# Kernel tuning notes

Measured on AMD Instinct MI355X. Metric: run time of the kernel, lower is better.

The kernel has to match this reference:

```python
import jax, jax.numpy as jnp
import numpy as np

N = 50000   # nodes
E = 800000  # edges
F = 64      # num_node_features
H = 64      # hidden_channels
NB = 3      # num_blocks
G = 64      # graphs in batch
C = 10      # num_classes
EPS = 1e-5  # BatchNorm eps


def setup_inputs() -> dict:
    key = jax.random.key(0)
    ks = jax.random.split(key, 24)
    x = jax.random.normal(ks[0], (N, F), dtype=jnp.float32)
    edge_index = jax.random.randint(ks[1], (2, E), 0, N, dtype=jnp.int64)
    batch = jnp.sort(jax.random.randint(ks[2], (N,), 0, G, dtype=jnp.int64))
    s = 0.05
    inp = {
        "x": x, "edge_index": edge_index, "batch": batch,
        "pre_w": jax.random.normal(ks[3], (F, H)) * s,
        "pre_b": jnp.zeros((H,), jnp.float32),
        # stacked per-block params (blocks are structurally identical)
        "blk_prelu1": jnp.full((NB,), 0.25, jnp.float32),
        "blk_bn_gamma": jnp.ones((NB, H), jnp.float32),
        "blk_bn_beta": jnp.zeros((NB, H), jnp.float32),
        "blk_w1": jax.random.normal(ks[4], (NB, H, 2 * H)) * s,
        "blk_b1": jnp.zeros((NB, 2 * H), jnp.float32),
        "blk_prelu2": jnp.full((NB,), 0.25, jnp.float32),
        "blk_w2": jax.random.normal(ks[5], (NB, 2 * H, H)) * s,
        "blk_b2": jnp.zeros((NB, H), jnp.float32),
        "post_bn_gamma": jnp.ones((H,), jnp.float32),
        "post_bn_beta": jnp.zeros((H,), jnp.float32),
        "fc1_w": jax.random.normal(ks[6], (H, 4 * H)) * s,
        "fc1_b": jnp.zeros((4 * H,), jnp.float32),
        "post_prelu": jnp.asarray(0.25, jnp.float32),
        "fc2_w": jax.random.normal(ks[7], (4 * H, C)) * s,
        "fc2_b": jnp.zeros((C,), jnp.float32),
    }
    return inp


def _prelu(x, a):
    return jnp.where(x >= 0, x, a * x)


def _batchnorm(x, gamma, beta):
    # training-mode BN over the node dimension (biased variance), as in torch
    mean = jnp.mean(x, axis=0)
    var = jnp.var(x, axis=0)
    return (x - mean) * jax.lax.rsqrt(var + EPS) * gamma + beta


def _gcn_conv(x, W, bias, src, dst):
    # PyG GCNConv: linear transform, then D^-1/2 (A+I) D^-1/2 aggregation, then bias.
    h = x @ W                                   # [N, out]
    deg = jax.ops.segment_sum(jnp.ones((E,), h.dtype), dst, num_segments=N) + 1.0
    dinv = jax.lax.rsqrt(deg)                   # [N]
    norm = dinv[src] * dinv[dst]                # [E]
    agg = jax.ops.segment_sum(h[src] * norm[:, None], dst, num_segments=N)
    agg = agg + h * (dinv * dinv)[:, None]      # self-loop contribution
    return agg + bias


def reference(x, edge_index, batch, pre_w, pre_b,
              blk_prelu1, blk_bn_gamma, blk_bn_beta, blk_w1, blk_b1,
              blk_prelu2, blk_w2, blk_b2,
              post_bn_gamma, post_bn_beta, fc1_w, fc1_b, post_prelu, fc2_w, fc2_b):
    src, dst = edge_index[0], edge_index[1]
    h = x @ pre_w + pre_b                       # [N, H]
    for i in range(NB):
        h = _prelu(h, blk_prelu1[i])
        h = _batchnorm(h, blk_bn_gamma[i], blk_bn_beta[i])
        h = _gcn_conv(h, blk_w1[i], blk_b1[i], src, dst)   # [N, 2H]
        h = _prelu(h, blk_prelu2[i])
        h = _gcn_conv(h, blk_w2[i], blk_b2[i], src, dst)   # [N, H]
    # global mean pool per graph
    sums = jax.ops.segment_sum(h, batch, num_segments=G)   # [G, H]
    cnts = jax.ops.segment_sum(jnp.ones((N,), h.dtype), batch, num_segments=G)
    pooled = sums / jnp.maximum(cnts, 1.0)[:, None]
    out = _batchnorm(pooled, post_bn_gamma, post_bn_beta)
    out = out @ fc1_w + fc1_b
    out = _prelu(out, post_prelu)
    # dropout with p=0.0 is identity
    out = out @ fc2_w + fc2_b                   # [G, C]
    return out
```

## Files before the change

### kernel.cpp

```cpp
#include <hip/hip_runtime.h>
#include <hip/hip_fp16.h>

#define NN 50000
#define NE 800000
#define NG 64
#define NC 10
#define BN_EPS 1e-5f
#define NSB 196

typedef __attribute__((ext_vector_type(2))) _Float16 h2v;
typedef __attribute__((ext_vector_type(8))) _Float16 f16x8;
typedef __attribute__((ext_vector_type(4))) float f32x4;

__device__ __forceinline__ float2 up2(unsigned u) {
    __half2 h = *reinterpret_cast<__half2*>(&u);
    return __half22float2(h);
}
__device__ __forceinline__ unsigned pk2(float a, float b) {
    __half2 h = __floats2half2_rn(a, b);
    return *reinterpret_cast<unsigned*>(&h);
}


__global__ void deg_count_kernel(const int* __restrict__ dst, int* __restrict__ deg,
                                 unsigned short* __restrict__ pos16) {
    int e = blockIdx.x * blockDim.x + threadIdx.x;
    if (e < NE) {
        int d = __builtin_nontemporal_load(&dst[e]);
        unsigned short p = (unsigned short)atomicAdd(&deg[d], 1);
        __builtin_nontemporal_store(p, &pos16[e]);
    }
}

__global__ __launch_bounds__(256) void block_sum_kernel(const int* __restrict__ deg,
                                                        int* __restrict__ bsum) {
    int b = blockIdx.x, t = threadIdx.x;
    int n = b * 256 + t;
    int v = (n < NN) ? deg[n] : 0;
    __shared__ int red[256];
    red[t] = v;
    __syncthreads();
    for (int off = 128; off > 0; off >>= 1) {
        if (t < off) red[t] += red[t + off];
        __syncthreads();
    }
    if (t == 0) bsum[b] = red[0];
}

__global__ __launch_bounds__(256) void bsum_scan_kernel(const int* __restrict__ bsum,
                                                        int* __restrict__ boff) {
    __shared__ int s[256];
    int t = threadIdx.x;
    int v = (t < NSB) ? bsum[t] : 0;
    s[t] = v;
    __syncthreads();
    for (int off = 1; off < 256; off <<= 1) {
        int cur = s[t];
        int add = (t >= off) ? s[t - off] : 0;
        __syncthreads();
        s[t] = cur + add;
        __syncthreads();
    }
    if (t < NSB) boff[t] = s[t] - v;
}

__global__ __launch_bounds__(256) void csr_setup_kernel(const int* __restrict__ deg,
                                                        const int* __restrict__ boff,
                                                        int* __restrict__ row_off,
                                                        float* __restrict__ dinv,
                                                        float* __restrict__ rdeg) {
    int b = blockIdx.x, t = threadIdx.x;
    int n = b * 256 + t;
    int v = (n < NN) ? deg[n] : 0;
    __shared__ int s[256];
    s[t] = v;
    __syncthreads();
    for (int off = 1; off < 256; off <<= 1) {
        int cur = s[t];
        int add = (t >= off) ? s[t - off] : 0;
        __syncthreads();
        s[t] = cur + add;
        __syncthreads();
    }
    int excl = s[t] - v + boff[b];
    if (n < NN) {
        row_off[n] = excl;
        float d = (float)v + 1.0f;
        dinv[n] = rsqrtf(d);
        rdeg[n] = sqrtf(d);
    }
    if (n == NN - 1) row_off[NN] = NE;
}

__global__ void scatter_pass_kernel(const int* __restrict__ src, const int* __restrict__ dst,
                                    const unsigned short* __restrict__ pos16,
                                    const int* __restrict__ row_off,
                                    int* __restrict__ csr_src, int d0, int d1) {
    int e = blockIdx.x * blockDim.x + threadIdx.x;
    if (e >= NE) return;
    int d = __builtin_nontemporal_load(&dst[e]);
    if (d < d0 || d >= d1) return;
    int s = __builtin_nontemporal_load(&src[e]);
    int p = (int)__builtin_nontemporal_load(&pos16[e]);
    csr_src[row_off[d] + p] = s;
}

__global__ void arow_kernel(const int* __restrict__ row_off, const int* __restrict__ csr_src,
                            const float* __restrict__ dinv, float* __restrict__ arow) {
    int n = blockIdx.x * 256 + threadIdx.x;
    if (n >= NN) return;
    float dv = dinv[n];
    float s = dv;
    int e0 = row_off[n], e1 = row_off[n + 1];
    for (int i = e0; i < e1; ++i) s += dinv[csr_src[i]];
    arow[n] = dv * s;
}


__global__ __launch_bounds__(256) void bn_stats_kernel(const __half* __restrict__ h,
                                                       const float* __restrict__ rdeg,
                                                       const float* __restrict__ alpha_p,
                                                       float* __restrict__ stats) {
    float alpha = alpha_p[0];
    int tid = threadIdx.x;
    int cg0 = tid & 7;
    int c8 = cg0 * 8;
    int rg = tid >> 3;
    float sm[8], sq[8];
#pragma unroll
    for (int k = 0; k < 8; ++k) { sm[k] = 0.f; sq[k] = 0.f; }
    for (int n = blockIdx.x * 32 + rg; n < NN; n += gridDim.x * 32) {
        float rd = rdeg[n];
        uint4 u = *(const uint4*)&h[(size_t)n * 64 + c8];
        float2 p0 = up2(u.x), p1 = up2(u.y), p2 = up2(u.z), p3 = up2(u.w);
        float e[8] = {p0.x, p0.y, p1.x, p1.y, p2.x, p2.y, p3.x, p3.y};
#pragma unroll
        for (int k = 0; k < 8; ++k) {
            float a = e[k] >= 0.f ? e[k] : alpha * e[k];
            a *= rd;
            sm[k] += a;
            sq[k] += a * a;
        }
    }
    __shared__ float ls[256 * 17];
    float* p = &ls[tid * 17];
#pragma unroll
    for (int k = 0; k < 8; ++k) { p[k] = sm[k]; p[8 + k] = sq[k]; }
    __syncthreads();
    if (tid < 128) {
        int cg = tid >> 4;
        int j = tid & 15;
        float acc = 0.f;
        for (int r = 0; r < 32; ++r) acc += ls[(r * 8 + cg) * 17 + j];
        int ch = cg * 8 + (j & 7);
        atomicAdd(&stats[(j < 8 ? 0 : 64) + ch], acc);
    }
}


template <bool PRELU, int OUT>
__global__ __launch_bounds__(256) void gather_kernel(const int* __restrict__ row_off,
                                                     const int* __restrict__ csr_src,
                                                     const float* __restrict__ dinv,
                                                     const float* __restrict__ bias,
                                                     const float* __restrict__ alpha_p,
                                                     const __half* __restrict__ hh,
                                                     __half* __restrict__ outp) {
    int tid = threadIdx.x;
    int r = blockIdx.x * 32 + (tid >> 3);
    int c = (tid & 7) * 8;
    if (r >= NN) return;
    float alpha = 0.f;
    if constexpr (PRELU) alpha = alpha_p[0];
    float acc[8];
    {
        uint4 u0 = *(const uint4*)&hh[(size_t)r * 64 + c];
        float2 p0 = up2(u0.x), p1 = up2(u0.y), p2 = up2(u0.z), p3 = up2(u0.w);
        acc[0] = p0.x; acc[1] = p0.y; acc[2] = p1.x; acc[3] = p1.y;
        acc[4] = p2.x; acc[5] = p2.y; acc[6] = p3.x; acc[7] = p3.y;
        if constexpr (PRELU) {
#pragma unroll
            for (int k = 0; k < 8; ++k) acc[k] = acc[k] >= 0.f ? acc[k] : alpha * acc[k];
        }
    }
    int beg = row_off[r];
    int end = row_off[r + 1];
    int nct = (end - beg + 7) >> 3;
    int base = beg;
    int q[8];
    if (nct > 0) {
#pragma unroll
        for (int j = 0; j < 8; ++j) {
            int pos = base + j;
            q[j] = csr_src[pos < end ? pos : end - 1];
        }
    }
    for (int it = 0; it < nct; ++it) {
        int s[8];
#pragma unroll
        for (int j = 0; j < 8; ++j) s[j] = q[j];
        int cbase = base;
        base += 8;
        if (it + 1 < nct) {
#pragma unroll
            for (int j = 0; j < 8; ++j) {
                int pos = base + j;
                q[j] = csr_src[pos < end ? pos : end - 1];
            }
        }
        uint4 v[8];
#pragma unroll
        for (int j = 0; j < 8; ++j) v[j] = *(const uint4*)&hh[(size_t)s[j] * 64 + c];
#pragma unroll
        for (int j = 0; j < 8; ++j) {
            float m = (cbase + j < end) ? 1.f : 0.f;
            float2 p0 = up2(v[j].x), p1 = up2(v[j].y), p2 = up2(v[j].z), p3 = up2(v[j].w);
            float e[8] = {p0.x, p0.y, p1.x, p1.y, p2.x, p2.y, p3.x, p3.y};
            if constexpr (PRELU) {
#pragma unroll
                for (int k = 0; k < 8; ++k) e[k] = e[k] >= 0.f ? e[k] : alpha * e[k];
            }
#pragma unroll
            for (int k = 0; k < 8; ++k) acc[k] = fmaf(e[k], m, acc[k]);
        }
    }
    float dv = dinv[r];
    float o[8];
    if constexpr (OUT == 2) {
#pragma unroll
        for (int k = 0; k < 8; ++k) o[k] = dv * acc[k];
    } else {
        float4 b0 = *(const float4*)&bias[c];
        float4 b1 = *(const float4*)&bias[c + 4];
        float bl[8] = {b0.x, b0.y, b0.z, b0.w, b1.x, b1.y, b1.z, b1.w};
#pragma unroll
        for (int k = 0; k < 8; ++k) o[k] = dv * acc[k] + bl[k];
        if constexpr (OUT == 1) {
#pragma unroll
            for (int k = 0; k < 8; ++k) o[k] *= dv;
        }
    }
    uint4 ov;
    ov.x = pk2(o[0], o[1]);
    ov.y = pk2(o[2], o[3]);
    ov.z = pk2(o[4], o[5]);
    ov.w = pk2(o[6], o[7]);
    *(uint4*)&outp[(size_t)r * 64 + c] = ov;
}


__global__ __launch_bounds__(256) void mfma_pre_kernel(const float* __restrict__ x,
                                                       const float* __restrict__ W,
                                                       __half* __restrict__ outp,
                                                       const float* __restrict__ bias,
                                                       const float* __restrict__ dinv) {
    __shared__ _Float16 At[128][72];
    __shared__ _Float16 Wt[64][72];
    int tid = threadIdx.x;
    for (int i = tid; i < 64 * 32; i += 256) {
        int j = i & 63;
        int k2 = i >> 6;
        *(unsigned*)&Wt[j][2 * k2] = pk2(W[(2 * k2) * 64 + j], W[(2 * k2 + 1) * 64 + j]);
    }
    int r0 = blockIdx.x * 128;
    for (int i = tid; i < 128 * 16; i += 256) {
        int row = i >> 4;
        int k4 = (i & 15) * 4;
        int rr = r0 + row;
        if (rr > NN - 1) rr = NN - 1;
        float4 v = *(const float4*)&x[(size_t)rr * 64 + k4];
        *(unsigned*)&At[row][k4]     = pk2(v.x, v.y);
        *(unsigned*)&At[row][k4 + 2] = pk2(v.z, v.w);
    }
    __syncthreads();
    int w = tid >> 6;
    int l = tid & 63;
    int lr = l & 15;
    int lk = (l >> 4) * 8;
    f32x4 acc[2][4];
#pragma unroll
    for (int rt = 0; rt < 2; ++rt)
#pragma unroll
        for (int ct = 0; ct < 4; ++ct) acc[rt][ct] = (f32x4){0.f, 0.f, 0.f, 0.f};
#pragma unroll
    for (int k0 = 0; k0 < 64; k0 += 32) {
        f16x8 a0 = *(const f16x8*)&At[w * 32 + lr][k0 + lk];
        f16x8 a1 = *(const f16x8*)&At[w * 32 + 16 + lr][k0 + lk];
#pragma unroll
        for (int ct = 0; ct < 4; ++ct) {
            f16x8 b = *(const f16x8*)&Wt[ct * 16 + lr][k0 + lk];
            acc[0][ct] = __builtin_amdgcn_mfma_f32_16x16x32_f16(a0, b, acc[0][ct], 0, 0, 0);
            acc[1][ct] = __builtin_amdgcn_mfma_f32_16x16x32_f16(a1, b, acc[1][ct], 0, 0, 0);
        }
    }
    int rowbase = r0 + w * 32 + (l >> 4) * 4;
#pragma unroll
    for (int rt = 0; rt < 2; ++rt) {
#pragma unroll
        for (int ct = 0; ct < 4; ++ct) {
            int col = ct * 16 + lr;
            float bb = bias[col];
#pragma unroll
            for (int r = 0; r < 4; ++r) {
                int row = rowbase + rt * 16 + r;
                if (row < NN)
                    outp[(size_t)row * 64 + col] = __float2half((acc[rt][ct][r] + bb) * dinv[row]);
            }
        }
    }
}


__global__ __launch_bounds__(256) void mfma_mlp_kernel(__half* __restrict__ t,
                                                       const float* __restrict__ W1,
                                                       const float* __restrict__ b1,
                                                       const float* __restrict__ W2,
                                                       const float* __restrict__ alpha2_p,
                                                       const float* __restrict__ stats,
                                                       const float* __restrict__ gamma,
                                                       const float* __restrict__ beta,
                                                       const float* __restrict__ arow,
                                                       const float* __restrict__ dinv) {
    __shared__ __align__(16) char smem[45056];
    auto Wt1 = (_Float16(*)[72])smem;
    auto Wt2 = (_Float16(*)[136])smem;
    auto At  = (_Float16(*)[72])(smem + 18432);
    auto Ut  = (_Float16(*)[136])(smem + 27648);
    __shared__ float scS[64], shS[64];
    int tid = threadIdx.x;
    if (tid < 64) {
        float mean = stats[tid] * (1.0f / NN);
        float var  = stats[64 + tid] * (1.0f / NN) - mean * mean;
        float sc = gamma[tid] * rsqrtf(var + BN_EPS);
        scS[tid] = sc;
        shS[tid] = beta[tid] - mean * sc;
    }
    for (int i = tid; i < 128 * 32; i += 256) {
        int j = i & 127;
        int k2 = i >> 7;
        *(unsigned*)&Wt1[j][2 * k2] = pk2(W1[(2 * k2) * 128 + j], W1[(2 * k2 + 1) * 128 + j]);
    }
    int r0 = blockIdx.x * 64;
    for (int i = tid; i < 64 * 16; i += 256) {
        int row = i >> 4;
        int k4 = (i & 15) * 4;
        int rr = r0 + row;
        if (rr > NN - 1) rr = NN - 1;
        uint2 uu = *(const uint2*)&t[(size_t)rr * 64 + k4];
        float2 lo = up2(uu.x), hi = up2(uu.y);
        float av = arow[rr];
        float vx = lo.x * scS[k4 + 0] + shS[k4 + 0] * av;
        float vy = lo.y * scS[k4 + 1] + shS[k4 + 1] * av;
        float vz = hi.x * scS[k4 + 2] + shS[k4 + 2] * av;
        float vw = hi.y * scS[k4 + 3] + shS[k4 + 3] * av;
        *(unsigned*)&At[row][k4]     = pk2(vx, vy);
        *(unsigned*)&At[row][k4 + 2] = pk2(vz, vw);
    }
    __syncthreads();
    int w = tid >> 6;
    int l = tid & 63;
    int lr = l & 15;
    int lk = (l >> 4) * 8;
    int rloc = w * 16 + (l >> 4) * 4;
    {
        f32x4 acc[8];
#pragma unroll
        for (int ct = 0; ct < 8; ++ct) acc[ct] = (f32x4){0.f, 0.f, 0.f, 0.f};
#pragma unroll
        for (int k0 = 0; k0 < 64; k0 += 32) {
            f16x8 a = *(const f16x8*)&At[w * 16 + lr][k0 + lk];
#pragma unroll
            for (int ct = 0; ct < 8; ++ct) {
                f16x8 b = *(const f16x8*)&Wt1[ct * 16 + lr][k0 + lk];
                acc[ct] = __builtin_amdgcn_mfma_f32_16x16x32_f16(a, b, acc[ct], 0, 0, 0);
            }
        }
        float alpha = alpha2_p[0];
#pragma unroll
        for (int ct = 0; ct < 8; ++ct) {
            int col = ct * 16 + lr;
            float bb = b1[col];
#pragma unroll
            for (int r = 0; r < 4; ++r) {
                float v = acc[ct][r] + bb;
                v = v >= 0.f ? v : alpha * v;
                Ut[rloc + r][col] = (_Float16)v;
            }
        }
    }
    __syncthreads();
    for (int i = tid; i < 64 * 64; i += 256) {
        int j = i & 63;
        int k2 = i >> 6;
        *(unsigned*)&Wt2[j][2 * k2] = pk2(W2[(2 * k2) * 64 + j], W2[(2 * k2 + 1) * 64 + j]);
    }
    __syncthreads();
    {
        f32x4 acc[4];
#pragma unroll
        for (int ct = 0; ct < 4; ++ct) acc[ct] = (f32x4){0.f, 0.f, 0.f, 0.f};
#pragma unroll
        for (int k0 = 0; k0 < 128; k0 += 32) {
            f16x8 a = *(const f16x8*)&Ut[w * 16 + lr][k0 + lk];
#pragma unroll
            for (int ct = 0; ct < 4; ++ct) {
                f16x8 b = *(const f16x8*)&Wt2[ct * 16 + lr][k0 + lk];
                acc[ct] = __builtin_amdgcn_mfma_f32_16x16x32_f16(a, b, acc[ct], 0, 0, 0);
            }
        }
#pragma unroll
        for (int ct = 0; ct < 4; ++ct) {
            int col = ct * 16 + lr;
#pragma unroll
            for (int r = 0; r < 4; ++r) {
                int row = r0 + rloc + r;
                if (row < NN) t[(size_t)row * 64 + col] = __float2half(acc[ct][r] * dinv[row]);
            }
        }
    }
}


__global__ __launch_bounds__(256) void pool_seg_kernel(const __half* __restrict__ h,
                                                       const int* __restrict__ batch,
                                                       float* __restrict__ pooled) {
    int g = blockIdx.x;
    __shared__ int sbeg, send;
    int tid = threadIdx.x;
    if (tid == 0) {
        int lo = 0, hi = NN;
        while (lo < hi) { int mid = (lo + hi) >> 1; if (batch[mid] < g) lo = mid + 1; else hi = mid; }
        sbeg = lo;
        lo = 0; hi = NN;
        while (lo < hi) { int mid = (lo + hi) >> 1; if (batch[mid] < g + 1) lo = mid + 1; else hi = mid; }
        send = lo;
    }
    __syncthreads();
    int beg = sbeg, end = send;
    int c4 = (tid & 15) * 4;
    int rg = tid >> 4;
    float sx = 0, sy = 0, sz = 0, sw = 0;
    for (int n = beg + rg; n < end; n += 16) {
        uint2 u = *(const uint2*)&h[(size_t)n * 64 + c4];
        float2 lo = up2(u.x), hi = up2(u.y);
        sx += lo.x; sy += lo.y; sz += hi.x; sw += hi.y;
    }
    __shared__ float red[256 * 4];
    float* p = &red[tid * 4];
    p[0] = sx; p[1] = sy; p[2] = sz; p[3] = sw;
    __syncthreads();
    if (tid < 64) {
        int cg = tid >> 2;
        int j = tid & 3;
        float acc = 0.f;
        for (int r = 0; r < 16; ++r) acc += red[(r * 16 + cg) * 4 + j];
        float cnt = fmaxf((float)(end - beg), 1.0f);
        pooled[g * 64 + cg * 4 + j] = acc / cnt;
    }
}


__global__ __launch_bounds__(64) void head_stats_kernel(const float* __restrict__ pooled,
                                                        const float* __restrict__ gamma,
                                                        const float* __restrict__ beta,
                                                        float* __restrict__ headsc) {
    int ch = threadIdx.x;
    float s = 0.f, q = 0.f;
    for (int g = 0; g < 64; ++g) {
        float v = pooled[g * 64 + ch];
        s += v; q += v * v;
    }
    float mean = s * (1.0f / 64.0f);
    float var = q * (1.0f / 64.0f) - mean * mean;
    float sc = gamma[ch] * rsqrtf(var + BN_EPS);
    headsc[ch] = sc;
    headsc[64 + ch] = beta[ch] - mean * sc;
}

__global__ __launch_bounds__(256) void head_fc_kernel(const float* __restrict__ pooled,
                                                      const float* __restrict__ headsc,
                                                      const float* __restrict__ fc1w,
                                                      const float* __restrict__ fc1b,
                                                      const float* __restrict__ prelu_p,
                                                      const float* __restrict__ fc2w,
                                                      const float* __restrict__ fc2b,
                                                      float* __restrict__ out) {
    int g = blockIdx.x;
    int tid = threadIdx.x;
    __shared__ float pr[64];
    __shared__ float red[256];
    if (tid < 64) pr[tid] = pooled[g * 64 + tid] * headsc[tid] + headsc[64 + tid];
    __syncthreads();
    float alpha = prelu_p[0];
    float o1 = fc1b[tid];
    for (int k = 0; k < 64; ++k) o1 += pr[k] * fc1w[k * 256 + tid];
    o1 = o1 >= 0.f ? o1 : alpha * o1;
    for (int c = 0; c < NC; ++c) {
        red[tid] = o1 * fc2w[tid * NC + c];
        __syncthreads();
        for (int off = 128; off > 0; off >>= 1) {
            if (tid < off) red[tid] += red[tid + off];
            __syncthreads();
        }
        if (tid == 0) out[g * NC + c] = red[0] + fc2b[c];
        __syncthreads();
    }
}


extern "C" void kernel_launch(void* const* d_in, const int* in_sizes, int n_in,
                              void* d_out, int out_size, void* d_ws, size_t ws_size,
                              hipStream_t stream) {
    const float* x       = (const float*)d_in[0];
    const int*   ei      = (const int*)d_in[1];
    const int*   batch   = (const int*)d_in[2];
    const float* pre_w   = (const float*)d_in[3];
    const float* pre_b   = (const float*)d_in[4];
    const float* bp1     = (const float*)d_in[5];
    const float* bng     = (const float*)d_in[6];
    const float* bnb     = (const float*)d_in[7];
    const float* bw1     = (const float*)d_in[8];
    const float* bb1     = (const float*)d_in[9];
    const float* bp2     = (const float*)d_in[10];
    const float* bw2     = (const float*)d_in[11];
    const float* bb2     = (const float*)d_in[12];
    const float* pgamma  = (const float*)d_in[13];
    const float* pbeta   = (const float*)d_in[14];
    const float* fc1w    = (const float*)d_in[15];
    const float* fc1b    = (const float*)d_in[16];
    const float* pprelu  = (const float*)d_in[17];
    const float* fc2w    = (const float*)d_in[18];
    const float* fc2b    = (const float*)d_in[19];

    const int* src = ei;
    const int* dst = ei + NE;

    __half* hA16 = (__half*)d_ws;
    __half* t16  = hA16 + (size_t)NN * 64;
    float* dinv  = (float*)(t16 + (size_t)NN * 64);
    float* rdeg  = dinv + NN;
    float* arow  = rdeg + NN;
    float* stats = arow + NN;
    int*   deg   = (int*)(stats + 3 * 128);
    float* pooledg = (float*)(deg + NN);
    float* headsc  = pooledg + 64 * 64;
    int*   csr_src = (int*)(headsc + 128);
    int*   row_off = csr_src + NE;
    int*   bsum    = row_off + NN + 1;
    int*   boff    = bsum + NSB;
    unsigned short* pos16 = (unsigned short*)(boff + NSB);

    hipMemsetAsync(stats, 0, ((size_t)3 * 128 + NN) * 4, stream);

    deg_count_kernel<<<(NE + 255) / 256, 256, 0, stream>>>(dst, deg, pos16);
    block_sum_kernel<<<NSB, 256, 0, stream>>>(deg, bsum);
    bsum_scan_kernel<<<1, 256, 0, stream>>>(bsum, boff);
    csr_setup_kernel<<<NSB, 256, 0, stream>>>(deg, boff, row_off, dinv, rdeg);
    for (int p = 0; p < 2; ++p) {
        int d0 = p * 25000;
        int d1 = (p == 1) ? NN : d0 + 25000;
        scatter_pass_kernel<<<(NE + 255) / 256, 256, 0, stream>>>(
            src, dst, pos16, row_off, csr_src, d0, d1);
    }
    arow_kernel<<<(NN + 255) / 256, 256, 0, stream>>>(row_off, csr_src, dinv, arow);

    mfma_pre_kernel<<<(NN + 127) / 128, 256, 0, stream>>>(x, pre_w, hA16, pre_b, dinv);

    int ggrid = (NN + 31) / 32;
    for (int i = 0; i < 3; ++i) {
        const float* a1 = bp1 + i;
        const float* a2 = bp2 + i;
        const float* gm = bng + i * 64;
        const float* bt = bnb + i * 64;
        const float* w1 = bw1 + (size_t)i * 64 * 128;
        const float* b1 = bb1 + i * 128;
        const float* w2 = bw2 + (size_t)i * 128 * 64;
        const float* b2 = bb2 + i * 64;
        float* st = stats + i * 128;

        bn_stats_kernel<<<512, 256, 0, stream>>>(hA16, rdeg, a1, st);
        gather_kernel<true, 2><<<ggrid, 256, 0, stream>>>(
            row_off, csr_src, dinv, nullptr, a1, hA16, t16);
        mfma_mlp_kernel<<<(NN + 63) / 64, 256, 0, stream>>>(
            t16, w1, b1, w2, a2, st, gm, bt, arow, dinv);
        if (i < 2) {
            gather_kernel<false, 1><<<ggrid, 256, 0, stream>>>(
                row_off, csr_src, dinv, b2, nullptr, t16, hA16);
        } else {
            gather_kernel<false, 0><<<ggrid, 256, 0, stream>>>(
                row_off, csr_src, dinv, b2, nullptr, t16, hA16);
        }
    }

    pool_seg_kernel<<<NG, 256, 0, stream>>>(hA16, batch, pooledg);
    head_stats_kernel<<<1, 64, 0, stream>>>(pooledg, pgamma, pbeta, headsc);
    head_fc_kernel<<<NG, 256, 0, stream>>>(pooledg, headsc, fc1w, fc1b, pprelu,
                                           fc2w, fc2b, (float*)d_out);
}
```

Baseline: 347.0 us.

## Fuse next-block BatchNorm statistics into gather epilogue and inline head stats

For blocks 0 and 1, the second aggregation kernel now computes the pre-scaled PReLU activations it already holds in registers and reduces per-channel sum and sum-of-squares through shared memory, with atomics into the next block's stats. This removes two separate bn_stats passes over the full feature matrix; only the first block's stats still run as a standalone kernel. The head BatchNorm statistics are now recomputed inside each head_fc block, which drops one tiny launch at the cost of redundant work. The gather kernel gains a 17KB shared buffer and a barrier, which may reduce occupancy. Out-of-range threads are now kept alive so they can take part in the barrier.

```diff
diff --git a/kernel.cpp b/kernel.cpp
--- a/kernel.cpp
+++ b/kernel.cpp
@@ -123,8 +123,7 @@
                                                        float* __restrict__ stats) {
     float alpha = alpha_p[0];
     int tid = threadIdx.x;
-    int cg0 = tid & 7;
-    int c8 = cg0 * 8;
+    int c8 = (tid & 7) * 8;
     int rg = tid >> 3;
     float sm[8], sq[8];
 #pragma unroll
@@ -158,23 +157,30 @@
 }
 
 
-template <bool PRELU, int OUT>
+template <bool PRELU, int OUT, bool STATS>
 __global__ __launch_bounds__(256) void gather_kernel(const int* __restrict__ row_off,
                                                      const int* __restrict__ csr_src,
                                                      const float* __restrict__ dinv,
                                                      const float* __restrict__ bias,
                                                      const float* __restrict__ alpha_p,
                                                      const __half* __restrict__ hh,
-                                                     __half* __restrict__ outp) {
+                                                     __half* __restrict__ outp,
+                                                     const float* __restrict__ alpha_s_p,
+                                                     float* __restrict__ stats) {
+    static_assert(!STATS || OUT == 1, "STATS requires OUT==1");
     int tid = threadIdx.x;
     int r = blockIdx.x * 32 + (tid >> 3);
     int c = (tid & 7) * 8;
-    if (r >= NN) return;
+    bool valid = r < NN;
+    if constexpr (!STATS) {
+        if (!valid) return;
+    }
+    int rr = valid ? r : 0;
     float alpha = 0.f;
     if constexpr (PRELU) alpha = alpha_p[0];
     float acc[8];
     {
-        uint4 u0 = *(const uint4*)&hh[(size_t)r * 64 + c];
+        uint4 u0 = *(const uint4*)&hh[(size_t)rr * 64 + c];
         float2 p0 = up2(u0.x), p1 = up2(u0.y), p2 = up2(u0.z), p3 = up2(u0.w);
         acc[0] = p0.x; acc[1] = p0.y; acc[2] = p1.x; acc[3] = p1.y;
         acc[4] = p2.x; acc[5] = p2.y; acc[6] = p3.x; acc[7] = p3.y;
@@ -183,8 +189,8 @@
             for (int k = 0; k < 8; ++k) acc[k] = acc[k] >= 0.f ? acc[k] : alpha * acc[k];
         }
     }
-    int beg = row_off[r];
-    int end = row_off[r + 1];
+    int beg = valid ? row_off[rr] : 0;
+    int end = valid ? row_off[rr + 1] : 0;
     int nct = (end - beg + 7) >> 3;
     int base = beg;
     int q[8];
@@ -224,7 +230,7 @@
             for (int k = 0; k < 8; ++k) acc[k] = fmaf(e[k], m, acc[k]);
         }
     }
-    float dv = dinv[r];
+    float dv = dinv[rr];
     float o[8];
     if constexpr (OUT == 2) {
 #pragma unroll
@@ -235,17 +241,40 @@
         float bl[8] = {b0.x, b0.y, b0.z, b0.w, b1.x, b1.y, b1.z, b1.w};
 #pragma unroll
         for (int k = 0; k < 8; ++k) o[k] = dv * acc[k] + bl[k];
+        if constexpr (STATS) {
+            float als = alpha_s_p[0];
+            __shared__ float ls[256 * 17];
+            float* p = &ls[tid * 17];
+#pragma unroll
+            for (int k = 0; k < 8; ++k) {
+                float u = valid ? o[k] : 0.f;
+                float sp = u >= 0.f ? u : als * u;
+                p[k] = sp;
+                p[8 + k] = sp * sp;
+            }
+            __syncthreads();
+            if (tid < 128) {
+                int cg = tid >> 4;
+                int j = tid & 15;
+                float accs = 0.f;
+                for (int rw = 0; rw < 32; ++rw) accs += ls[(rw * 8 + cg) * 17 + j];
+                int ch = cg * 8 + (j & 7);
+                atomicAdd(&stats[(j < 8 ? 0 : 64) + ch], accs);
+            }
+        }
         if constexpr (OUT == 1) {
 #pragma unroll
             for (int k = 0; k < 8; ++k) o[k] *= dv;
         }
     }
-    uint4 ov;
-    ov.x = pk2(o[0], o[1]);
-    ov.y = pk2(o[2], o[3]);
-    ov.z = pk2(o[4], o[5]);
-    ov.w = pk2(o[6], o[7]);
-    *(uint4*)&outp[(size_t)r * 64 + c] = ov;
+    if (valid) {
+        uint4 ov;
+        ov.x = pk2(o[0], o[1]);
+        ov.y = pk2(o[2], o[3]);
+        ov.z = pk2(o[4], o[5]);
+        ov.w = pk2(o[6], o[7]);
+        *(uint4*)&outp[(size_t)r * 64 + c] = ov;
+    }
 }
 
 
@@ -460,25 +489,9 @@
 }
 
 
-__global__ __launch_bounds__(64) void head_stats_kernel(const float* __restrict__ pooled,
-                                                        const float* __restrict__ gamma,
-                                                        const float* __restrict__ beta,
-                                                        float* __restrict__ headsc) {
-    int ch = threadIdx.x;
-    float s = 0.f, q = 0.f;
-    for (int g = 0; g < 64; ++g) {
-        float v = pooled[g * 64 + ch];
-        s += v; q += v * v;
-    }
-    float mean = s * (1.0f / 64.0f);
-    float var = q * (1.0f / 64.0f) - mean * mean;
-    float sc = gamma[ch] * rsqrtf(var + BN_EPS);
-    headsc[ch] = sc;
-    headsc[64 + ch] = beta[ch] - mean * sc;
-}
-
 __global__ __launch_bounds__(256) void head_fc_kernel(const float* __restrict__ pooled,
-                                                      const float* __restrict__ headsc,
+                                                      const float* __restrict__ gamma,
+                                                      const float* __restrict__ beta,
                                                       const float* __restrict__ fc1w,
                                                       const float* __restrict__ fc1b,
                                                       const float* __restrict__ prelu_p,
@@ -489,7 +502,17 @@
     int tid = threadIdx.x;
     __shared__ float pr[64];
     __shared__ float red[256];
-    if (tid < 64) pr[tid] = pooled[g * 64 + tid] * headsc[tid] + headsc[64 + tid];
+    if (tid < 64) {
+        float s = 0.f, q = 0.f;
+        for (int gg = 0; gg < 64; ++gg) {
+            float v = pooled[gg * 64 + tid];
+            s += v; q += v * v;
+        }
+        float mean = s * (1.0f / 64.0f);
+        float var = q * (1.0f / 64.0f) - mean * mean;
+        float sc = gamma[tid] * rsqrtf(var + BN_EPS);
+        pr[tid] = pooled[g * 64 + tid] * sc + (beta[tid] - mean * sc);
+    }
     __syncthreads();
     float alpha = prelu_p[0];
     float o1 = fc1b[tid];
@@ -543,8 +566,7 @@
     float* stats = arow + NN;
     int*   deg   = (int*)(stats + 3 * 128);
     float* pooledg = (float*)(deg + NN);
-    float* headsc  = pooledg + 64 * 64;
-    int*   csr_src = (int*)(headsc + 128);
+    int*   csr_src = (int*)(pooledg + 64 * 64);
     int*   row_off = csr_src + NE;
     int*   bsum    = row_off + NN + 1;
     int*   boff    = bsum + NSB;
@@ -565,6 +587,8 @@
     arow_kernel<<<(NN + 255) / 256, 256, 0, stream>>>(row_off, csr_src, dinv, arow);
 
     mfma_pre_kernel<<<(NN + 127) / 128, 256, 0, stream>>>(x, pre_w, hA16, pre_b, dinv);
+
+    bn_stats_kernel<<<512, 256, 0, stream>>>(hA16, rdeg, bp1, stats);
 
     int ggrid = (NN + 31) / 32;
     for (int i = 0; i < 3; ++i) {
@@ -578,22 +602,21 @@
         const float* b2 = bb2 + i * 64;
         float* st = stats + i * 128;
 
-        bn_stats_kernel<<<512, 256, 0, stream>>>(hA16, rdeg, a1, st);
-        gather_kernel<true, 2><<<ggrid, 256, 0, stream>>>(
-            row_off, csr_src, dinv, nullptr, a1, hA16, t16);
+        gather_kernel<true, 2, false><<<ggrid, 256, 0, stream>>>(
+            row_off, csr_src, dinv, nullptr, a1, hA16, t16, nullptr, nullptr);
         mfma_mlp_kernel<<<(NN + 63) / 64, 256, 0, stream>>>(
             t16, w1, b1, w2, a2, st, gm, bt, arow, dinv);
         if (i < 2) {
-            gather_kernel<false, 1><<<ggrid, 256, 0, stream>>>(
-                row_off, csr_src, dinv, b2, nullptr, t16, hA16);
+            gather_kernel<false, 1, true><<<ggrid, 256, 0, stream>>>(
+                row_off, csr_src, dinv, b2, nullptr, t16, hA16,
+                bp1 + (i + 1), stats + (i + 1) * 128);
         } else {
-            gather_kernel<false, 0><<<ggrid, 256, 0, stream>>>(
-                row_off, csr_src, dinv, b2, nullptr, t16, hA16);
+            gather_kernel<false, 0, false><<<ggrid, 256, 0, stream>>>(
+                row_off, csr_src, dinv, b2, nullptr, t16, hA16, nullptr, nullptr);
         }
     }
 
     pool_seg_kernel<<<NG, 256, 0, stream>>>(hA16, batch, pooledg);
-    head_stats_kernel<<<1, 64, 0, stream>>>(pooledg, pgamma, pbeta, headsc);
-    head_fc_kernel<<<NG, 256, 0, stream>>>(pooledg, headsc, fc1w, fc1b, pprelu,
+    head_fc_kernel<<<NG, 256, 0, stream>>>(pooledg, pgamma, pbeta, fc1w, fc1b, pprelu,
                                            fc2w, fc2b, (float*)d_out);
 }
```

Result: slower. 379.9 us (+9.5%).
